# Kernel tuning notes

Hardware: AMD Instinct MI355X
Metric: run time of the kernel (lower is better)

Reference implementation:

```python
import jax, jax.numpy as jnp
import numpy as np

DIM = 768
H = 6        # pinned by router mask construction (3 logits -> 6 head gates)
HD = DIM // H  # 128
TAU = 5.0

def setup_inputs() -> dict:
    key = jax.random.key(0)
    ks = jax.random.split(key, 10)
    w = 0.02
    return {
        "x": jax.random.normal(ks[0], (4, 2048, DIM), jnp.float32),
        "latency": jax.random.uniform(ks[1], (1,), jnp.float32),
        "qkv_w": jax.random.normal(ks[2], (3 * DIM, DIM), jnp.float32) * w,
        "qkv_b": jax.random.normal(ks[3], (3 * DIM,), jnp.float32) * w,
        "proj_w": jax.random.normal(ks[4], (DIM, DIM), jnp.float32) * w,
        "proj_b": jax.random.normal(ks[5], (DIM,), jnp.float32) * w,
        "router_w": jax.random.normal(ks[6], (3, 1), jnp.float32),
        "router_b": jax.random.normal(ks[7], (3,), jnp.float32),
        # gumbel noise g = -log(Exp(1)), matching -empty.exponential_().log()
        "g1": -jnp.log(jax.random.exponential(ks[8], (3,), jnp.float32)),
        "g2": -jnp.log(jax.random.exponential(ks[9], (3,), jnp.float32)),
    }

def reference(x, latency, qkv_w, qkv_b, proj_w, proj_b, router_w, router_b, g1, g2):
    # router: Linear(1, 3) on scalar latency -> 3 logits
    logits = router_w @ latency + router_b                      # [3]
    # gumbel-sigmoid, tau=5, hard=True with straight-through estimator
    y_soft = jax.nn.sigmoid((logits + g1 - g2) / TAU)           # [3]
    y_hard = (y_soft > 0.5).astype(y_soft.dtype)
    mask3 = y_hard - jax.lax.stop_gradient(y_soft) + y_soft     # [3]
    # first logit gates 4 heads, remaining two gate one head each -> 6 heads
    mask6 = jnp.concatenate([mask3[:1], mask3[:1], mask3[:1], mask3])  # [6]
    maskC = jnp.repeat(mask6, HD)                               # [DIM]

    B, N, C = x.shape
    qkv = jnp.einsum('bnc,oc->bno', x, qkv_w) + qkv_b           # [B,N,3*DIM]
    qkv = qkv.reshape(B, N, 3, H, HD)
    q, k, v = qkv[:, :, 0], qkv[:, :, 1], qkv[:, :, 2]          # [B,N,H,HD]

    scale = HD ** -0.5
    attn = jax.nn.softmax(jnp.einsum('bqhd,bkhd->bhqk', q * scale, k), axis=-1)
    out = jnp.einsum('bhqk,bkhd->bqhd', attn, v).reshape(B, N, C)

    out = out * maskC                                            # gate heads/channels
    return jnp.einsum('bnc,oc->bno', out, proj_w) + proj_b
```

## Files before the change

kernel.cpp:

```cpp
#include <hip/hip_runtime.h>
#include <cstdint>

#define DIM_ 768
#define H_ 6
#define HD_ 128
#define NB_ 4
#define SEQ_ 2048
#define TOK_ (NB_*SEQ_)
#define OUT3_ (3*DIM_)
#define L2E 1.4426950408889634f

typedef __bf16 bf16;
typedef __bf16 bf16x4 __attribute__((ext_vector_type(4)));
typedef __bf16 bf16x8 __attribute__((ext_vector_type(8)));
typedef float f32x4 __attribute__((ext_vector_type(4)));
typedef float f32x16 __attribute__((ext_vector_type(16)));
typedef unsigned int u32;
typedef u32 u32x4 __attribute__((ext_vector_type(4)));

__device__ __forceinline__ void gload16(const void* g, void* lds) {
  __builtin_amdgcn_global_load_lds((const __attribute__((address_space(1))) void*)g,
                                   (__attribute__((address_space(3))) void*)lds,
                                   16, 0, 0);
}

__global__ void prep_kernel(const float* __restrict__ x, const float* __restrict__ qw,
                            const float* __restrict__ pw,
                            const float* __restrict__ latency, const float* __restrict__ rw,
                            const float* __restrict__ rb, const float* __restrict__ g1,
                            const float* __restrict__ g2,
                            bf16* __restrict__ xb, bf16* __restrict__ wqb,
                            bf16* __restrict__ wpb, float* __restrict__ mask6) {
  if (blockIdx.x == 0 && threadIdx.x < 6) {
    int i = threadIdx.x;
    int j = (i < 4) ? 0 : (i - 3);
    float logit = rw[j] * latency[0] + rb[j];
    float z = (logit + g1[j] - g2[j]) / 5.0f;
    float ys = 1.0f / (1.0f + expf(-z));
    float yh = ys > 0.5f ? 1.0f : 0.0f;
    mask6[i] = (yh - ys) + ys;
  }
  const int QX  = TOK_ * DIM_ / 4;
  const int QWQ = OUT3_ * DIM_ / 4;
  int gid = blockIdx.x * 256 + threadIdx.x;
  const float* src;
  bf16* dst;
  int off;
  if (gid < QX) { src = x; dst = xb; off = gid; }
  else if (gid < QX + QWQ) { src = qw; dst = wqb; off = gid - QX; }
  else { src = pw; dst = wpb; off = gid - QX - QWQ; }
  float4 v = *reinterpret_cast<const float4*>(src + off * 4);
  bf16x4 o = { (bf16)v.x, (bf16)v.y, (bf16)v.z, (bf16)v.w };
  *reinterpret_cast<bf16x4*>(dst + off * 4) = o;
}


__global__ __launch_bounds__(256)
void qkv_gemm(const bf16* __restrict__ A, const bf16* __restrict__ W,
              const float* __restrict__ bias, const float* __restrict__ mask6,
              bf16* __restrict__ q, bf16* __restrict__ k, bf16* __restrict__ vt) {
  __shared__ bf16 AB[2][8192];
  bf16* Frag = &AB[0][0];
  const int tid = threadIdx.x;
  const int l = tid & 63, w = tid >> 6;
  const int lr = l & 15, lg = l >> 4;
  const int wm = w >> 1, wn = w & 1;
  const int tm = blockIdx.y * 128;
  const int on = blockIdx.x * 128;

  const int sblk = (on < DIM_) ? 0 : (on < 2 * DIM_ ? 1 : 2);
  const int hblk = (on - sblk * DIM_) >> 7;
  if (mask6[hblk] == 0.0f) return;

  const int lrow = l >> 2;
  const int scol = ((l & 3) ^ (lrow & 3)) * 8;

  f32x4 acc[4][4];
#pragma unroll
  for (int i = 0; i < 4; ++i)
#pragma unroll
    for (int j = 0; j < 4; ++j) acc[i][j] = f32x4{0.f, 0.f, 0.f, 0.f};

  auto STAGE = [&](int k0, int buf) {
#pragma unroll
    for (int u = 0; u < 2; ++u) {
      int rbase = w * 32 + u * 16;
      gload16(A + (size_t)(tm + rbase + lrow) * DIM_ + k0 + scol, &AB[buf][rbase * 32]);
      gload16(W + (size_t)(on + rbase + lrow) * DIM_ + k0 + scol, &AB[buf][4096 + rbase * 32]);
    }
  };

  STAGE(0, 0);
  __syncthreads();
  for (int t = 0; t < 24; ++t) {
    if (t + 1 < 24) STAGE((t + 1) * 32, (t + 1) & 1);
    const bf16* As = &AB[t & 1][0];
    const bf16* Bs = &AB[t & 1][4096];
    bf16x8 af[4], bfr[4];
#pragma unroll
    for (int i = 0; i < 4; ++i) {
      int row = wm * 64 + i * 16 + lr;
      af[i] = *reinterpret_cast<const bf16x8*>(As + row * 32 + ((lg ^ (row & 3)) * 8));
    }
#pragma unroll
    for (int j = 0; j < 4; ++j) {
      int row = wn * 64 + j * 16 + lr;
      bfr[j] = *reinterpret_cast<const bf16x8*>(Bs + row * 32 + ((lg ^ (row & 3)) * 8));
    }
#pragma unroll
    for (int i = 0; i < 4; ++i)
#pragma unroll
      for (int j = 0; j < 4; ++j)
        acc[i][j] = __builtin_amdgcn_mfma_f32_16x16x32_bf16(af[i], bfr[j], acc[i][j], 0, 0, 0);
    __syncthreads();
  }

  const int n0 = tm & 2047;
  const int bb = tm >> 11;
  const int bhh = bb * H_ + hblk;

  if (on < 2 * DIM_) {
    const int s = sblk;
    const float scale = 0.08838834764831845f * L2E;
    bf16* dstbase = (s == 0) ? q : k;
#pragma unroll
    for (int i = 0; i < 4; ++i) {
#pragma unroll
      for (int j = 0; j < 4; ++j) {
        int dd = wn * 64 + j * 16 + lr;
        int kc = dd >> 4, hi8 = (dd >> 3) & 1, e = dd & 7;
        float bia = bias[on + dd];
#pragma unroll
        for (int r = 0; r < 4; ++r) {
          int nl = wm * 64 + i * 16 + lg * 4 + r;
          float val = acc[i][j][r] + bia;
          if (s == 0) val *= scale;
          Frag[(((nl >> 5) * 8 + kc) << 9) + ((hi8 * 32 + (nl & 31)) << 3) + e] = (bf16)val;
        }
      }
    }
    __syncthreads();
    size_t base = ((size_t)bhh * 64 + (n0 >> 5)) * 4096;
#pragma unroll
    for (int it = 0; it < 8; ++it) {
      int idx = it * 2048 + tid * 8;
      bf16x8 v8 = *reinterpret_cast<const bf16x8*>(Frag + idx);
      *reinterpret_cast<bf16x8*>(dstbase + base + idx) = v8;
    }
  } else {
    bf16(*Ts)[136] = reinterpret_cast<bf16(*)[136]>(Frag);
    for (int wc = 0; wc < 2; ++wc) {
      __syncthreads();
      if (wn == wc) {
#pragma unroll
        for (int j = 0; j < 4; ++j) {
          float bia = bias[on + wc * 64 + j * 16 + lr];
#pragma unroll
          for (int i = 0; i < 4; ++i) {
            bf16x4 pk;
#pragma unroll
            for (int r = 0; r < 4; ++r) pk[r] = (bf16)(acc[i][j][r] + bia);
            *reinterpret_cast<bf16x4*>(&Ts[j * 16 + lr][wm * 64 + i * 16 + lg * 4]) = pk;
          }
        }
      }
      __syncthreads();
#pragma unroll
      for (int it = 0; it < 4; ++it) {
        int row = it * 16 + (tid >> 4);
        int c8 = (tid & 15) * 8;
        bf16x8 v8 = *reinterpret_cast<const bf16x8*>(&Ts[row][c8]);
        int d = wc * 64 + row;
        int n = n0 + c8;
        size_t idx = (((((size_t)bhh * 32 + (n >> 6)) * 4 + ((n >> 4) & 3)) * 4 + (d >> 5)) << 9) +
                     ((((n >> 3) & 1) * 32 + (d & 31)) << 3);
        *reinterpret_cast<bf16x8*>(vt + idx) = v8;
      }
    }
  }
}

__global__ __launch_bounds__(256)
void proj_gemm(const bf16* __restrict__ A, const bf16* __restrict__ W,
               const float* __restrict__ bias, float* __restrict__ out) {
  __shared__ bf16 AB[2][12288];
  const int tid = threadIdx.x;
  const int l = tid & 63, w = tid >> 6;
  const int lr = l & 15, lg = l >> 4;
  const int wm = w >> 1, wn = w & 1;
  const int tm = blockIdx.y * 128;
  const int on = blockIdx.x * 64;

  const int lrow = l >> 3;
  const int scol = ((l & 7) ^ lrow) * 8;

  f32x4 acc[4][2];
#pragma unroll
  for (int i = 0; i < 4; ++i)
#pragma unroll
    for (int j = 0; j < 2; ++j) acc[i][j] = f32x4{0.f, 0.f, 0.f, 0.f};

  auto STAGE = [&](int k0, int buf) {
#pragma unroll
    for (int u = 0; u < 4; ++u) {
      int br = w * 32 + u * 8;
      gload16(A + (size_t)(tm + br + lrow) * DIM_ + k0 + scol, &AB[buf][br * 64]);
    }
#pragma unroll
    for (int u = 0; u < 2; ++u) {
      int br = w * 16 + u * 8;
      gload16(W + (size_t)(on + br + lrow) * DIM_ + k0 + scol, &AB[buf][8192 + br * 64]);
    }
  };

  STAGE(0, 0);
  __syncthreads();
  for (int t = 0; t < 12; ++t) {
    if (t + 1 < 12) STAGE((t + 1) * 64, (t + 1) & 1);
    const bf16* As = &AB[t & 1][0];
    const bf16* Bs = &AB[t & 1][8192];
#pragma unroll
    for (int kk = 0; kk < 2; ++kk) {
      bf16x8 af[4], bfr[2];
#pragma unroll
      for (int i = 0; i < 4; ++i) {
        int row = wm * 64 + i * 16 + lr;
        af[i] = *reinterpret_cast<const bf16x8*>(As + row * 64 + (((kk << 2) + lg) ^ (row & 7)) * 8);
      }
#pragma unroll
      for (int j = 0; j < 2; ++j) {
        int row = wn * 32 + j * 16 + lr;
        bfr[j] = *reinterpret_cast<const bf16x8*>(Bs + row * 64 + (((kk << 2) + lg) ^ (row & 7)) * 8);
      }
#pragma unroll
      for (int i = 0; i < 4; ++i)
#pragma unroll
        for (int j = 0; j < 2; ++j)
          acc[i][j] = __builtin_amdgcn_mfma_f32_16x16x32_bf16(af[i], bfr[j], acc[i][j], 0, 0, 0);
    }
    __syncthreads();
  }

#pragma unroll
  for (int i = 0; i < 4; ++i) {
#pragma unroll
    for (int j = 0; j < 2; ++j) {
      int o = on + wn * 32 + j * 16 + lr;
      float bia = bias[o];
#pragma unroll
      for (int r = 0; r < 4; ++r) {
        int t = tm + wm * 64 + i * 16 + lg * 4 + r;
        out[(size_t)t * DIM_ + o] = acc[i][j][r] + bia;
      }
    }
  }
}

__global__ __launch_bounds__(128, 2)
void attn_kernel(const bf16* __restrict__ qf_g, const bf16* __restrict__ kf_g,
                 const bf16* __restrict__ vf_g, const float* __restrict__ mask6,
                 bf16* __restrict__ ab) {
  __shared__ char smem[16640];

  const int tid = threadIdx.x;
  const int l = tid & 63;
  const int w = tid >> 6;
  const int kl = l & 31, hi = l >> 5;
  const int bid = blockIdx.x;
  const int bh = bid % 24;
  const int qt = bid / 24;
  const int h = bh % H_;
  const int b = bh / H_;
  const int q0 = qt * 32;
  const int loff = l * 8;
  const float hm = mask6[h];

  if (hm == 0.0f) {
    bf16x8 z = __builtin_bit_cast(bf16x8, u32x4{0u, 0u, 0u, 0u});
    int row = tid >> 2, c0 = (tid & 3) * 32;
    bf16* dst = ab + ((size_t)b * SEQ_ + q0 + row) * DIM_ + h * HD_ + c0;
#pragma unroll
    for (int u = 0; u < 4; ++u)
      *reinterpret_cast<bf16x8*>(dst + u * 8) = z;
    return;
  }

  float* OM  = (float*)smem;
  float* MLm = (float*)(smem + 16384);
  float* MLl = MLm + 32;

  const bf16* qq = qf_g + (((size_t)bh * 64 + qt) * 8) * 512;
  const bf16* kq = kf_g + (size_t)bh * 262144 + (size_t)w * 32 * 4096;
  const bf16* vq = vf_g + (size_t)bh * 262144 + (size_t)w * 32 * 4096;

  bf16x8 qf[8];
#pragma unroll
  for (int kc = 0; kc < 8; ++kc)
    qf[kc] = *reinterpret_cast<const bf16x8*>(qq + kc * 512 + loff);

  f32x16 oacc[4];
#pragma unroll
  for (int df = 0; df < 4; ++df)
#pragma unroll
    for (int r = 0; r < 16; ++r) oacc[df][r] = 0.f;
  float m_lane = -3.0e38f;
  float lsum = 0.f;

  for (int jj = 0; jj < 32; ++jj) {
    const bf16* kb = kq + (size_t)jj * 4096;
    const bf16* vb = vq + (size_t)jj * 4096;

    f32x16 sacc;
#pragma unroll
    for (int r = 0; r < 16; ++r) sacc[r] = 0.f;
    __builtin_amdgcn_s_setprio(1);
#pragma unroll
    for (int kc = 0; kc < 8; ++kc) {
      bf16x8 kfr = *reinterpret_cast<const bf16x8*>(kb + kc * 512 + loff);
      sacc = __builtin_amdgcn_mfma_f32_32x32x16_bf16(kfr, qf[kc], sacc, 0, 0, 0);
    }
    __builtin_amdgcn_s_setprio(0);

    float t = sacc[0];
#pragma unroll
    for (int r = 1; r < 16; ++r) t = fmaxf(t, sacc[r]);
    t = fmaxf(t, __shfl_xor(t, 32));
    bool need = t > m_lane + 8.0f;
    if (__ballot(need) != 0ull) {
      float nm = fmaxf(m_lane, t);
      float c = exp2f(m_lane - nm);
      m_lane = nm;
      lsum *= c;
#pragma unroll
      for (int r = 0; r < 16; ++r) {
        float cr = __shfl(c, (r & 3) + 8 * (r >> 2) + 4 * hi);
#pragma unroll
        for (int df = 0; df < 4; ++df) oacc[df][r] *= cr;
      }
    }

    u32 pp[8];
#pragma unroll
    for (int m = 0; m < 8; ++m) {
      float e0 = exp2f(sacc[2 * m] - m_lane);
      float e1 = exp2f(sacc[2 * m + 1] - m_lane);
      lsum += e0 + e1;
      union { u32 u; bf16 hh2[2]; } pk;
      pk.hh2[0] = (bf16)e0; pk.hh2[1] = (bf16)e1;
      pp[m] = pk.u;
    }

    u32x4 afv[2];
#pragma unroll
    for (int ks = 0; ks < 2; ++ks) {
#pragma unroll
      for (int i = 0; i < 2; ++i) {
        u32 a = pp[4 * ks + i];
        u32 b2 = pp[4 * ks + 2 + i];
        asm volatile("v_permlane32_swap_b32 %0, %1" : "+v"(a), "+v"(b2));
        afv[ks][i] = a;
        afv[ks][2 + i] = b2;
      }
    }

    __builtin_amdgcn_s_setprio(1);
#pragma unroll
    for (int ks = 0; ks < 2; ++ks) {
      bf16x8 pa = __builtin_bit_cast(bf16x8, afv[ks]);
#pragma unroll
      for (int df = 0; df < 4; ++df) {
        bf16x8 vfr = *reinterpret_cast<const bf16x8*>(vb + (ks * 4 + df) * 512 + loff);
        oacc[df] = __builtin_amdgcn_mfma_f32_32x32x16_bf16(pa, vfr, oacc[df], 0, 0, 0);
      }
    }
    __builtin_amdgcn_s_setprio(0);
  }

  float lt = lsum + __shfl_xor(lsum, 32);

  if (w == 1) {
#pragma unroll
    for (int r = 0; r < 16; ++r) {
      int qloc = (r & 3) + 8 * (r >> 2) + 4 * hi;
#pragma unroll
      for (int df = 0; df < 4; ++df)
        OM[qloc * 128 + df * 32 + kl] = oacc[df][r];
    }
    MLm[kl] = m_lane;
    MLl[kl] = lt;
  }
  __syncthreads();
  if (w == 1) return;

  float m1 = MLm[kl];
  float l1 = MLl[kl];
  float M = fmaxf(m_lane, m1);
  float a0 = exp2f(m_lane - M), a1 = exp2f(m1 - M);
  float L = lt * a0 + l1 * a1;
  float s0 = a0 * hm / L, s1 = a1 * hm / L;

#pragma unroll
  for (int r = 0; r < 16; ++r) {
    int qloc = (r & 3) + 8 * (r >> 2) + 4 * hi;
    float r0 = __shfl(s0, qloc);
    float r1 = __shfl(s1, qloc);
    int n = q0 + qloc;
#pragma unroll
    for (int df = 0; df < 4; ++df) {
      int d = df * 32 + kl;
      float o1 = OM[qloc * 128 + df * 32 + kl];
      ab[((size_t)b * SEQ_ + n) * DIM_ + h * HD_ + d] =
          (bf16)(oacc[df][r] * r0 + o1 * r1);
    }
  }
}

extern "C" void kernel_launch(void* const* d_in, const int* in_sizes, int n_in,
                              void* d_out, int out_size, void* d_ws, size_t ws_size,
                              hipStream_t stream) {
  const float* x        = (const float*)d_in[0];
  const float* latency  = (const float*)d_in[1];
  const float* qkv_w    = (const float*)d_in[2];
  const float* qkv_b    = (const float*)d_in[3];
  const float* proj_w   = (const float*)d_in[4];
  const float* proj_b   = (const float*)d_in[5];
  const float* router_w = (const float*)d_in[6];
  const float* router_b = (const float*)d_in[7];
  const float* g1       = (const float*)d_in[8];
  const float* g2       = (const float*)d_in[9];
  float* out = (float*)d_out;

  const size_t N_X  = (size_t)TOK_ * DIM_;
  const size_t N_WQ = (size_t)OUT3_ * DIM_;
  const size_t N_WP = (size_t)DIM_ * DIM_;
  const size_t N_P  = (size_t)NB_ * H_ * SEQ_ * HD_;

  float* maskp = (float*)d_ws;
  bf16* xb  = (bf16*)((char*)d_ws + 256);
  bf16* wqb = xb + N_X;
  bf16* wpb = wqb + N_WQ;
  bf16* qbf = wpb + N_WP;
  bf16* kbf = qbf + N_P;
  bf16* vtb = kbf + N_P;
  bf16* abf = vtb + N_P;

  size_t need = 256 + 2 * (N_X + N_WQ + N_WP + 4 * N_P);
  if (ws_size < need) return;

  const int prep_blocks = (int)((N_X + N_WQ + N_WP) / 1024);
  prep_kernel<<<prep_blocks, 256, 0, stream>>>(x, qkv_w, proj_w, latency, router_w,
                                               router_b, g1, g2, xb, wqb, wpb, maskp);

  qkv_gemm<<<dim3(OUT3_ / 128, TOK_ / 128), 256, 0, stream>>>(xb, wqb, qkv_b, maskp, qbf, kbf, vtb);
  attn_kernel<<<dim3(24 * (SEQ_ / 32)), 128, 0, stream>>>(qbf, kbf, vtb, maskp, abf);
  proj_gemm<<<dim3(DIM_ / 64, TOK_ / 128), 256, 0, stream>>>(abf, wpb, proj_b, out);
}
```

Before: 171.5 us.

## Triple-buffer GEMM K-loop with vmcnt waits and single barrier per step

Both QKV and projection GEMMs move from double-buffered LDS staging with two __syncthreads per iteration to a three-stage ring buffer. Each step waits on vmcnt for the oldest async global->LDS load, then issues one barrier. Prefetch runs two K-steps ahead to hide global load latency. The projection GEMM also drops its K-tile from 64 to 32 (24 steps), matching the QKV layout and cutting LDS use, at the cost of more loop iterations and barriers.

```diff
diff --git a/kernel.cpp b/kernel.cpp
--- a/kernel.cpp
+++ b/kernel.cpp
@@ -59,7 +59,7 @@
 void qkv_gemm(const bf16* __restrict__ A, const bf16* __restrict__ W,
               const float* __restrict__ bias, const float* __restrict__ mask6,
               bf16* __restrict__ q, bf16* __restrict__ k, bf16* __restrict__ vt) {
-  __shared__ bf16 AB[2][8192];
+  __shared__ bf16 AB[3][8192];
   bf16* Frag = &AB[0][0];
   const int tid = threadIdx.x;
   const int l = tid & 63, w = tid >> 6;
@@ -91,11 +91,15 @@
   };
 
   STAGE(0, 0);
-  __syncthreads();
+  STAGE(32, 1);
   for (int t = 0; t < 24; ++t) {
-    if (t + 1 < 24) STAGE((t + 1) * 32, (t + 1) & 1);
-    const bf16* As = &AB[t & 1][0];
-    const bf16* Bs = &AB[t & 1][4096];
+    if (t < 23) asm volatile("s_waitcnt vmcnt(4)" ::: "memory");
+    else        asm volatile("s_waitcnt vmcnt(0)" ::: "memory");
+    __builtin_amdgcn_s_barrier();
+    if (t + 2 < 24) STAGE((t + 2) * 32, (t + 2) % 3);
+
+    const bf16* As = &AB[t % 3][0];
+    const bf16* Bs = &AB[t % 3][4096];
     bf16x8 af[4], bfr[4];
 #pragma unroll
     for (int i = 0; i < 4; ++i) {
@@ -112,7 +116,6 @@
 #pragma unroll
       for (int j = 0; j < 4; ++j)
         acc[i][j] = __builtin_amdgcn_mfma_f32_16x16x32_bf16(af[i], bfr[j], acc[i][j], 0, 0, 0);
-    __syncthreads();
   }
 
   const int n0 = tm & 2047;
@@ -123,6 +126,7 @@
     const int s = sblk;
     const float scale = 0.08838834764831845f * L2E;
     bf16* dstbase = (s == 0) ? q : k;
+    __syncthreads();
 #pragma unroll
     for (int i = 0; i < 4; ++i) {
 #pragma unroll
@@ -183,7 +187,7 @@
 __global__ __launch_bounds__(256)
 void proj_gemm(const bf16* __restrict__ A, const bf16* __restrict__ W,
                const float* __restrict__ bias, float* __restrict__ out) {
-  __shared__ bf16 AB[2][12288];
+  __shared__ bf16 AB[3][6144];
   const int tid = threadIdx.x;
   const int l = tid & 63, w = tid >> 6;
   const int lr = l & 15, lg = l >> 4;
@@ -191,8 +195,8 @@
   const int tm = blockIdx.y * 128;
   const int on = blockIdx.x * 64;
 
-  const int lrow = l >> 3;
-  const int scol = ((l & 7) ^ lrow) * 8;
+  const int lrow = l >> 2;
+  const int scol = ((l & 3) ^ (lrow & 3)) * 8;
 
   f32x4 acc[4][2];
 #pragma unroll
@@ -202,43 +206,40 @@
 
   auto STAGE = [&](int k0, int buf) {
 #pragma unroll
-    for (int u = 0; u < 4; ++u) {
-      int br = w * 32 + u * 8;
-      gload16(A + (size_t)(tm + br + lrow) * DIM_ + k0 + scol, &AB[buf][br * 64]);
-    }
-#pragma unroll
     for (int u = 0; u < 2; ++u) {
-      int br = w * 16 + u * 8;
-      gload16(W + (size_t)(on + br + lrow) * DIM_ + k0 + scol, &AB[buf][8192 + br * 64]);
-    }
+      int rbase = w * 32 + u * 16;
+      gload16(A + (size_t)(tm + rbase + lrow) * DIM_ + k0 + scol, &AB[buf][rbase * 32]);
+    }
+    int rbase = w * 16;
+    gload16(W + (size_t)(on + rbase + lrow) * DIM_ + k0 + scol, &AB[buf][4096 + rbase * 32]);
   };
 
   STAGE(0, 0);
-  __syncthreads();
-  for (int t = 0; t < 12; ++t) {
-    if (t + 1 < 12) STAGE((t + 1) * 64, (t + 1) & 1);
-    const bf16* As = &AB[t & 1][0];
-    const bf16* Bs = &AB[t & 1][8192];
-#pragma unroll
-    for (int kk = 0; kk < 2; ++kk) {
-      bf16x8 af[4], bfr[2];
-#pragma unroll
-      for (int i = 0; i < 4; ++i) {
-        int row = wm * 64 + i * 16 + lr;
-        af[i] = *reinterpret_cast<const bf16x8*>(As + row * 64 + (((kk << 2) + lg) ^ (row & 7)) * 8);
-      }
-#pragma unroll
-      for (int j = 0; j < 2; ++j) {
-        int row = wn * 32 + j * 16 + lr;
-        bfr[j] = *reinterpret_cast<const bf16x8*>(Bs + row * 64 + (((kk << 2) + lg) ^ (row & 7)) * 8);
-      }
-#pragma unroll
-      for (int i = 0; i < 4; ++i)
-#pragma unroll
-        for (int j = 0; j < 2; ++j)
-          acc[i][j] = __builtin_amdgcn_mfma_f32_16x16x32_bf16(af[i], bfr[j], acc[i][j], 0, 0, 0);
-    }
-    __syncthreads();
+  STAGE(32, 1);
+  for (int t = 0; t < 24; ++t) {
+    if (t < 23) asm volatile("s_waitcnt vmcnt(3)" ::: "memory");
+    else        asm volatile("s_waitcnt vmcnt(0)" ::: "memory");
+    __builtin_amdgcn_s_barrier();
+    if (t + 2 < 24) STAGE((t + 2) * 32, (t + 2) % 3);
+
+    const bf16* As = &AB[t % 3][0];
+    const bf16* Bs = &AB[t % 3][4096];
+    bf16x8 af[4], bfr[2];
+#pragma unroll
+    for (int i = 0; i < 4; ++i) {
+      int row = wm * 64 + i * 16 + lr;
+      af[i] = *reinterpret_cast<const bf16x8*>(As + row * 32 + ((lg ^ (row & 3)) * 8));
+    }
+#pragma unroll
+    for (int j = 0; j < 2; ++j) {
+      int row = wn * 32 + j * 16 + lr;
+      bfr[j] = *reinterpret_cast<const bf16x8*>(Bs + row * 32 + ((lg ^ (row & 3)) * 8));
+    }
+#pragma unroll
+    for (int i = 0; i < 4; ++i)
+#pragma unroll
+      for (int j = 0; j < 2; ++j)
+        acc[i][j] = __builtin_amdgcn_mfma_f32_16x16x32_bf16(af[i], bfr[j], acc[i][j], 0, 0, 0);
   }
 
 #pragma unroll
```

Result: no change. 173.2 us (+1.0%).
